# Kernel tuning notes

Measured on AMD Instinct MI355X. Metric: run time of the kernel, lower is better.

The kernel has to match this reference:

```python
import jax, jax.numpy as jnp
import numpy as np

N, M = 4096, 8192
NFEAT, EFEAT, NHID, NCLASS = 128, 64, 64, 16
ALPHA = 0.2
NEG = -9e15
BN_SCALE = np.float32(1.0 / np.sqrt(1.0 + 1e-5))  # eval BatchNorm: running stats (0,1), affine (1,0)


def _masked_att(hs, hd, a, mask):
    # hs: [P,F], hd: [Q,F], a: [2F], mask: [P,Q] binary
    F_ = hs.shape[1]
    logits = (hs @ a[:F_])[:, None] + (hd @ a[F_:])[None, :]            # [P,Q]
    logits = jnp.where(mask > 0, jax.nn.leaky_relu(logits, ALPHA), NEG)
    return jax.nn.softmax(logits, axis=1) @ hd                           # [P,F]


def _gat_layer(x, ex, adj, eadj, nem, Wn, We, ann, ane, aee, aen, concat):
    h = x @ Wn                                  # [N,F]
    g = ex @ We                                 # [M,F]
    Hn = _masked_att(h, h, ann, adj)            # node <- node neighbors
    He = _masked_att(h, g, ane, nem)            # node <- incident edges
    Ge = _masked_att(g, g, aee, eadj)           # edge <- adjacent edges
    Gn = _masked_att(g, h, aen, nem.T)          # edge <- endpoint nodes
    if concat:
        return (jax.nn.elu(jnp.concatenate([Hn, He], axis=1)),
                jax.nn.elu(jnp.concatenate([Ge, Gn], axis=1)))
    return Hn + He, Ge + Gn


def _mlp(h, W1, b1, W2, b2):
    h = jax.nn.relu((h @ W1 + b1) * BN_SCALE)
    return h @ W2 + b2


def _next_layer(h, A, W1, b1, W2, b2):
    pooled = A @ h                              # spmm(adj, h), dense-stored
    rep = _mlp(pooled, W1, b1, W2, b2)
    return jax.nn.relu(rep * BN_SCALE)


def setup_inputs() -> dict:
    key = jax.random.key(0)
    ks = jax.random.split(key, 40)
    f32 = jnp.float32
    x = jax.random.normal(ks[0], (N, NFEAT), f32)
    e_x = jax.random.normal(ks[1], (M, EFEAT), f32)
    adj = jnp.minimum((jax.random.uniform(ks[2], (N, N)) < 16.0 / N).astype(f32) + jnp.eye(N, dtype=f32), 1.0)
    e_adj = jnp.minimum((jax.random.uniform(ks[3], (M, M)) < 16.0 / M).astype(f32) + jnp.eye(M, dtype=f32), 1.0)
    n_e_adj = (jax.random.uniform(ks[4], (N, M)) < 4.0 / M).astype(f32)

    def lin(k, i, o):
        return jax.random.normal(k, (i, o), f32) * np.float32(1.0 / np.sqrt(i))

    def avec(k, F_):
        return jax.random.normal(k, (2 * F_,), f32) * np.float32(0.1)

    d = dict(x=x, e_x=e_x, adj=adj, e_adj=e_adj, n_e_adj=n_e_adj)
    # layer dims: (node_in, edge_in, out)
    dims = [(NFEAT, EFEAT, NHID), (2 * NHID, 2 * NHID, 2 * NHID), (64, 64, NCLASS)]
    ki = 5
    for li, (ni, ei, fo) in enumerate(dims):
        d[f'l{li}_Wn'] = lin(ks[ki], ni, fo); ki += 1
        d[f'l{li}_We'] = lin(ks[ki], ei, fo); ki += 1
        for nm in ('ann', 'ane', 'aee', 'aen'):
            d[f'l{li}_{nm}'] = avec(ks[ki], fo); ki += 1
    mdims = [(256, 64, 64), (64, 64, 64)]
    for mi, (i_, h_, o_) in enumerate(mdims):
        d[f'm{mi}_W1'] = lin(ks[ki], i_, h_); ki += 1
        d[f'm{mi}_b1'] = jnp.zeros((h_,), f32)
        d[f'm{mi}_W2'] = lin(ks[ki], h_, o_); ki += 1
        d[f'm{mi}_b2'] = jnp.zeros((o_,), f32)
    return d


def reference(x, e_x, adj, e_adj, n_e_adj,
              l0_Wn, l0_We, l0_ann, l0_ane, l0_aee, l0_aen,
              l1_Wn, l1_We, l1_ann, l1_ane, l1_aee, l1_aen,
              l2_Wn, l2_We, l2_ann, l2_ane, l2_aee, l2_aen,
              m0_W1, m0_b1, m0_W2, m0_b2,
              m1_W1, m1_b1, m1_W2, m1_b2):
    # dropout is identity in eval mode
    h, g = _gat_layer(x, e_x, adj, e_adj, n_e_adj, l0_Wn, l0_We, l0_ann, l0_ane, l0_aee, l0_aen, True)
    h, g = _gat_layer(h, g, adj, e_adj, n_e_adj, l1_Wn, l1_We, l1_ann, l1_ane, l1_aee, l1_aen, True)
    h_n, h_e = h, g
    h_n = _next_layer(h_n, adj, m0_W1, m0_b1, m0_W2, m0_b2)
    h_n = _next_layer(h_n, adj, m1_W1, m1_b1, m1_W2, m1_b2)
    h_e = _next_layer(h_e, e_adj, m0_W1, m0_b1, m0_W2, m0_b2)
    h_e = _next_layer(h_e, e_adj, m1_W1, m1_b1, m1_W2, m1_b2)
    fn, fe = _gat_layer(h_n, h_e, adj, e_adj, n_e_adj, l2_Wn, l2_We, l2_ann, l2_ane, l2_aee, l2_aen, False)
    return (jax.nn.log_softmax(jax.nn.elu(fn), axis=1),
            jax.nn.log_softmax(jax.nn.elu(fe), axis=1))
```

## Files before the change

### kernel.cpp

```cpp
#include <hip/hip_runtime.h>
#include <cmath>

constexpr int N_ = 4096;
constexpr int M_ = 8192;
constexpr float ALPHA_ = 0.2f;
constexpr float BN_SC = 0.9999950000374998f;
constexpr int CAP = 64;

typedef unsigned long long u64;

__device__ __forceinline__ float lrelu(float x) { return x > 0.f ? x : ALPHA_ * x; }
__device__ __forceinline__ float elu(float x) { return x > 0.f ? x : __expf(x) - 1.f; }

struct CsrA {
  const float* adj; const float* eadj; const float* nem;
  int* cA; int* iA; int* cE; int* iE; int* cN; int* iN; int* cT; int* iT;
};

__device__ void csr_body(const CsrA& a) {
  int wid = blockIdx.x * 8 + (threadIdx.x >> 6);
  int lane = threadIdx.x & 63;
  const float* mask; int row, Q; int* cnt; int* idx; bool tr = false;
  if (wid < N_)           { mask = a.adj;  row = wid;            Q = N_; cnt = a.cA; idx = a.iA; }
  else if (wid < N_ + M_) { mask = a.eadj; row = wid - N_;       Q = M_; cnt = a.cE; idx = a.iE; }
  else                    { mask = a.nem;  row = wid - N_ - M_;  Q = M_; cnt = a.cN; idx = a.iN; tr = true; }
  const float* mr = mask + (size_t)row * Q;
  u64 lt = (1ull << lane) - 1ull;
  int total = 0;
  for (int q0 = 0; q0 < Q; q0 += 256) {
    float4 v = *reinterpret_cast<const float4*>(mr + q0 + lane * 4);
    unsigned mk = (v.x > 0.5f ? 1u : 0u) | (v.y > 0.5f ? 2u : 0u) |
                  (v.z > 0.5f ? 4u : 0u) | (v.w > 0.5f ? 8u : 0u);
    u64 b0 = __ballot(mk & 1u), b1 = __ballot(mk & 2u), b2 = __ballot(mk & 4u), b3 = __ballot(mk & 8u);
    if (mk) {
      int base = total + __popcll(b0 & lt) + __popcll(b1 & lt) + __popcll(b2 & lt) + __popcll(b3 & lt);
      int ob = 0;
#pragma unroll
      for (int e = 0; e < 4; e++) {
        if (mk & (1u << e)) {
          int pos = base + ob;
          int j = q0 + lane * 4 + e;
          if (pos < CAP) idx[(size_t)row * CAP + pos] = j;
          if (tr) {
            int tp = atomicAdd(&a.cT[j], 1);
            if (tp < CAP) a.iT[(size_t)j * CAP + tp] = row;
          }
          ob++;
        }
      }
    }
    total += __popcll(b0) + __popcll(b1) + __popcll(b2) + __popcll(b3);
  }
  if (lane == 0) cnt[row] = min(total, CAP);
}

struct PDOp {
  const float* X; const float* W; int K, P;
  const float* a0; const float* a1; const float* a2; const float* a3;
  float* o0; float* o1; float* o2; float* o3;
  float* Y;
};

template <int F>
__device__ void proj_body(const PDOp& op, float* part) {
  constexpr int RPB = 512 / F;
  constexpr int KC = 8192 / F;
  __shared__ float Wl[8192];
  __shared__ float dred[8][4];
  int rl = threadIdx.x / F;
  int f = threadIdx.x % F;
  int p = blockIdx.x * RPB + rl;
  bool act = p < op.P;
  float acc = 0.f;
  for (int k0 = 0; k0 < op.K; k0 += KC) {
    int kc = min(KC, op.K - k0);
    __syncthreads();
    for (int i = threadIdx.x; i < kc * F; i += 512) Wl[i] = op.W[(size_t)k0 * F + i];
    __syncthreads();
    if (act) {
      const float4* xr4 = reinterpret_cast<const float4*>(op.X + (size_t)p * op.K + k0);
      for (int k = 0; k < kc; k += 4) {
        float4 xv = xr4[k >> 2];
        acc = fmaf(xv.x, Wl[k * F + f], acc);
        acc = fmaf(xv.y, Wl[(k + 1) * F + f], acc);
        acc = fmaf(xv.z, Wl[(k + 2) * F + f], acc);
        acc = fmaf(xv.w, Wl[(k + 3) * F + f], acc);
      }
    }
  }
  if (act) op.Y[(size_t)p * F + f] = acc;
  float q0 = acc * op.a0[f];
  float q1 = acc * op.a1[f];
  float q2 = acc * op.a2[f];
  float q3 = acc * op.a3[f];
  constexpr int WID = F < 64 ? F : 64;
#pragma unroll
  for (int t = 1; t < WID; t <<= 1) {
    q0 += __shfl_xor(q0, t, WID);
    q1 += __shfl_xor(q1, t, WID);
    q2 += __shfl_xor(q2, t, WID);
    q3 += __shfl_xor(q3, t, WID);
  }
  if constexpr (F == 128) {
    int w = threadIdx.x >> 6;
    if ((threadIdx.x & 63) == 0) { dred[w][0] = q0; dred[w][1] = q1; dred[w][2] = q2; dred[w][3] = q3; }
    __syncthreads();
    if (act && f == 0) {
      int w0 = rl * 2;
      op.o0[p] = dred[w0][0] + dred[w0 + 1][0];
      op.o1[p] = dred[w0][1] + dred[w0 + 1][1];
      op.o2[p] = dred[w0][2] + dred[w0 + 1][2];
      op.o3[p] = dred[w0][3] + dred[w0 + 1][3];
    }
  } else {
    if (act && f == 0) { op.o0[p] = q0; op.o1[p] = q1; op.o2[p] = q2; op.o3[p] = q3; }
  }
  float* sred = Wl;
  __syncthreads();
  sred[rl * F + f] = act ? acc : 0.f;
  __syncthreads();
  if (rl == 0) {
    float s = 0.f;
    for (int r = 0; r < RPB; r++) s += sred[r * F + f];
    part[(size_t)blockIdx.x * F + f] = s;
  }
}

__global__ __launch_bounds__(512) void phase0(CsrA ca, PDOp A, PDOp B,
                                              float* partH, float* partG) {
  if (blockIdx.y == 0) { csr_body(ca); return; }
  if (blockIdx.x >= 1024) return;
  if (blockIdx.y == 1) proj_body<64>(A, partH);
  else                 proj_body<64>(B, partG);
}

template <int F>
__global__ __launch_bounds__(512) void proj_l(PDOp A, PDOp B, float* partH, float* partG) {
  if (blockIdx.y == 0) proj_body<F>(A, partH);
  else                 proj_body<F>(B, partG);
}

template <int F>
__global__ __launch_bounds__(1024) void part_reduce(const float* __restrict__ partH,
                                                    const float* __restrict__ partG,
                                                    int nb,
                                                    float* __restrict__ oh, float* __restrict__ og) {
  constexpr int SL = 1024 / F;
  const float* part = blockIdx.y ? partG : partH;
  float* o = blockIdx.y ? og : oh;
  int f = threadIdx.x % F;
  int w = threadIdx.x / F;
  float s = 0.f;
  int b = w;
  for (; b + 8 * SL <= nb; b += 8 * SL) {
    float v0 = part[(size_t)(b + 0 * SL) * F + f];
    float v1 = part[(size_t)(b + 1 * SL) * F + f];
    float v2 = part[(size_t)(b + 2 * SL) * F + f];
    float v3 = part[(size_t)(b + 3 * SL) * F + f];
    float v4 = part[(size_t)(b + 4 * SL) * F + f];
    float v5 = part[(size_t)(b + 5 * SL) * F + f];
    float v6 = part[(size_t)(b + 6 * SL) * F + f];
    float v7 = part[(size_t)(b + 7 * SL) * F + f];
    s += ((v0 + v1) + (v2 + v3)) + ((v4 + v5) + (v6 + v7));
  }
  for (; b < nb; b += SL) s += part[(size_t)b * F + f];
  __shared__ float red[1024];
  red[threadIdx.x] = s;
  __syncthreads();
  if (w == 0) {
    float t = 0.f;
#pragma unroll
    for (int ww = 0; ww < SL; ww++) t += red[ww * F + f];
    o[f] = t;
  }
}

struct AOp {
  const int* cnt; int* idx; const float* s; const float* d;
  const float* Hd; const float* cs; float* out; int ldo, ocol, P, Q;
  int sortL; int* cTw;
};

template <int F>
__global__ __launch_bounds__(256) void att4(AOp A0, AOp A1, AOp A2, AOp A3) {
  int y = blockIdx.y;
  AOp op = y == 0 ? A0 : y == 1 ? A1 : y == 2 ? A2 : A3;
  constexpr int C = F / 64;
  int row = blockIdx.x * 4 + (threadIdx.x >> 6);
  int lane = threadIdx.x & 63;
  if (row >= op.P) return;
  int n = min(op.cnt[row], CAP);
  float acc[C];
  if (n == 0) {
    float invQ = 1.f / (float)op.Q;
#pragma unroll
    for (int c = 0; c < C; c++) acc[c] = op.cs[lane + c * 64] * invQ;
  } else {
    float sp = op.s[row];
    int* ip = op.idx + (size_t)row * CAP;
    int jl;
    if (op.sortL) {
      int v = lane < n ? ip[lane] : 0x7fffffff;
#pragma unroll
      for (int k = 2; k <= 64; k <<= 1) {
#pragma unroll
        for (int s = k >> 1; s > 0; s >>= 1) {
          int o = __shfl_xor(v, s);
          bool keepmin = (((lane & s) == 0) == ((lane & k) == 0));
          v = keepmin ? min(v, o) : max(v, o);
        }
      }
      if (lane < n) ip[lane] = v;
      if (lane == 0) op.cTw[row] = n;
      jl = lane < n ? v : 0;
    } else {
      jl = lane < n ? ip[lane] : 0;
    }
    float dl = lane < n ? op.d[jl] : -INFINITY;
    float mm = dl;
#pragma unroll
    for (int t = 1; t < 64; t <<= 1) mm = fmaxf(mm, __shfl_xor(mm, t));
    float m = lrelu(sp + mm);
    float el = lane < n ? __expf(lrelu(sp + dl) - m) : 0.f;
    float l = el;
#pragma unroll
    for (int t = 1; t < 64; t <<= 1) l += __shfl_xor(l, t);
    float invl = 1.f / l;
#pragma unroll
    for (int c = 0; c < C; c++) acc[c] = 0.f;
    int k = 0;
    for (; k + 2 <= n; k += 2) {
      int j0 = __shfl(jl, k), j1 = __shfl(jl, k + 1);
      float e0 = __shfl(el, k), e1 = __shfl(el, k + 1);
      const float* h0 = op.Hd + (size_t)j0 * F + lane;
      const float* h1 = op.Hd + (size_t)j1 * F + lane;
#pragma unroll
      for (int c = 0; c < C; c++) acc[c] = fmaf(e0, h0[c * 64], fmaf(e1, h1[c * 64], acc[c]));
    }
    if (k < n) {
      int j0 = __shfl(jl, k);
      float e0 = __shfl(el, k);
#pragma unroll
      for (int c = 0; c < C; c++) acc[c] = fmaf(e0, op.Hd[(size_t)j0 * F + lane + c * 64], acc[c]);
    }
#pragma unroll
    for (int c = 0; c < C; c++) acc[c] *= invl;
  }
  float* o = op.out + (size_t)row * op.ldo + op.ocol + lane;
#pragma unroll
  for (int c = 0; c < C; c++) o[c * 64] = elu(acc[c]);
}

template <int C>
__global__ __launch_bounds__(256) void nextlayer(
    const int* __restrict__ cA, const int* __restrict__ iA,
    const int* __restrict__ cE, const int* __restrict__ iE,
    const float* __restrict__ HdN, const float* __restrict__ HdM,
    const float* __restrict__ W1, const float* __restrict__ b1,
    const float* __restrict__ W2, const float* __restrict__ b2,
    float* __restrict__ outN, float* __restrict__ outM) {
  constexpr int KD = C * 64;
  int y = blockIdx.y;
  const int* cnt = y ? cE : cA;
  const int* idx = y ? iE : iA;
  const float* Hd = y ? HdM : HdN;
  float* out = y ? outM : outN;
  int P = y ? M_ : N_;
  int w = threadIdx.x >> 6, lane = threadIdx.x & 63;
  int row = blockIdx.x * 4 + w;
  if (row >= P) return;
  int n = min(cnt[row], CAP);
  const int* ip = idx + (size_t)row * CAP;
  int jl = lane < n ? ip[lane] : 0;
  float acc[C];
#pragma unroll
  for (int c = 0; c < C; c++) acc[c] = 0.f;
  int k = 0;
  for (; k + 2 <= n; k += 2) {
    int j0 = __shfl(jl, k), j1 = __shfl(jl, k + 1);
    const float* h0 = Hd + (size_t)j0 * KD + lane;
    const float* h1 = Hd + (size_t)j1 * KD + lane;
#pragma unroll
    for (int c = 0; c < C; c++) acc[c] += h0[c * 64] + h1[c * 64];
  }
  if (k < n) {
    int j0 = __shfl(jl, k);
#pragma unroll
    for (int c = 0; c < C; c++) acc[c] += Hd[(size_t)j0 * KD + lane + c * 64];
  }
  float y1 = 0.f;
#pragma unroll
  for (int c = 0; c < C; c++) {
    for (int kk = 0; kk < 64; kk++)
      y1 = fmaf(__shfl(acc[c], kk), W1[(c * 64 + kk) * 64 + lane], y1);
  }
  y1 = fmaxf((y1 + b1[lane]) * BN_SC, 0.f);
  float y2 = 0.f;
  for (int kk = 0; kk < 64; kk++)
    y2 = fmaf(__shfl(y1, kk), W2[kk * 64 + lane], y2);
  out[(size_t)row * 64 + lane] = fmaxf((y2 + b2[lane]) * BN_SC, 0.f);
}

__device__ __forceinline__ float att_col16(const int* cnt, const int* idx, float sp,
                                           const float* d, const float* Hd,
                                           const float* cs, int Q, int row, int c) {
  int n = min(cnt[row], CAP);
  if (n == 0) return cs[c] / (float)Q;
  const int* ip = idx + (size_t)row * CAP;
  float mm = -INFINITY;
  for (int k0 = 0; k0 < n; k0 += 16) {
    int k = k0 + c;
    float dv = k < n ? d[ip[k]] : -INFINITY;
    mm = fmaxf(mm, dv);
  }
#pragma unroll
  for (int t = 1; t < 16; t <<= 1) mm = fmaxf(mm, __shfl_xor(mm, t, 16));
  float m = lrelu(sp + mm);
  float l = 0.f, a = 0.f;
  for (int k0 = 0; k0 < n; k0 += 16) {
    int k = k0 + c;
    int jx = k < n ? ip[k] : 0;
    float dv = k < n ? d[jx] : 0.f;
    float ex = k < n ? __expf(lrelu(sp + dv) - m) : 0.f;
    int kmax = min(16, n - k0);
    for (int kk = 0; kk < kmax; kk++) {
      float e = __shfl(ex, kk, 16);
      int j = __shfl(jx, kk, 16);
      l += e;
      a = fmaf(e, Hd[(size_t)j * 16 + c], a);
    }
  }
  return a / l;
}

__global__ __launch_bounds__(256) void att_final(
    const int* __restrict__ cA, const int* __restrict__ iA, const float* __restrict__ s0, const float* __restrict__ d0,
    const int* __restrict__ cN, const int* __restrict__ iN, const float* __restrict__ s1, const float* __restrict__ d1,
    const int* __restrict__ cE, const int* __restrict__ iE, const float* __restrict__ s2, const float* __restrict__ d2,
    const int* __restrict__ cT, const int* __restrict__ iT, const float* __restrict__ s3, const float* __restrict__ d3,
    const float* __restrict__ h2, const float* __restrict__ g2,
    const float* __restrict__ csh, const float* __restrict__ csg,
    float* __restrict__ out) {
  int y = blockIdx.y;
  int gid = blockIdx.x * 256 + threadIdx.x;
  int row = gid >> 4, c = gid & 15;
  float v; float* dst;
  if (y == 0) {
    if (row >= N_) return;
    v = att_col16(cA, iA, s0[row], d0, h2, csh, N_, row, c)
      + att_col16(cN, iN, s1[row], d1, g2, csg, M_, row, c);
    dst = out + (size_t)row * 16 + c;
  } else {
    if (row >= M_) return;
    v = att_col16(cE, iE, s2[row], d2, g2, csg, M_, row, c)
      + att_col16(cT, iT, s3[row], d3, h2, csh, N_, row, c);
    dst = out + (size_t)(N_ + row) * 16 + c;
  }
  v = elu(v);
  float mx = v;
#pragma unroll
  for (int t = 1; t < 16; t <<= 1) mx = fmaxf(mx, __shfl_xor(mx, t, 16));
  float ex = __expf(v - mx);
  float sm = ex;
#pragma unroll
  for (int t = 1; t < 16; t <<= 1) sm += __shfl_xor(sm, t, 16);
  *dst = v - mx - __logf(sm);
}

extern "C" void kernel_launch(void* const* d_in, const int* in_sizes, int n_in,
                              void* d_out, int out_size, void* d_ws, size_t ws_size,
                              hipStream_t stream) {
  (void)in_sizes; (void)n_in; (void)out_size; (void)ws_size;
  const float* x    = (const float*)d_in[0];
  const float* e_x  = (const float*)d_in[1];
  const float* adj  = (const float*)d_in[2];
  const float* eadj = (const float*)d_in[3];
  const float* nem  = (const float*)d_in[4];
  const float* l_Wn[3]  = {(const float*)d_in[5],  (const float*)d_in[11], (const float*)d_in[17]};
  const float* l_We[3]  = {(const float*)d_in[6],  (const float*)d_in[12], (const float*)d_in[18]};
  const float* l_ann[3] = {(const float*)d_in[7],  (const float*)d_in[13], (const float*)d_in[19]};
  const float* l_ane[3] = {(const float*)d_in[8],  (const float*)d_in[14], (const float*)d_in[20]};
  const float* l_aee[3] = {(const float*)d_in[9],  (const float*)d_in[15], (const float*)d_in[21]};
  const float* l_aen[3] = {(const float*)d_in[10], (const float*)d_in[16], (const float*)d_in[22]};
  const float* m_W1[2] = {(const float*)d_in[23], (const float*)d_in[27]};
  const float* m_b1[2] = {(const float*)d_in[24], (const float*)d_in[28]};
  const float* m_W2[2] = {(const float*)d_in[25], (const float*)d_in[29]};
  const float* m_b2[2] = {(const float*)d_in[26], (const float*)d_in[30]};
  float* outp = (float*)d_out;

  char* wsp = (char*)d_ws;
  size_t off = 0;
  auto alloc = [&](size_t bytes) -> void* {
    void* p = wsp + off;
    off += (bytes + 255) & ~(size_t)255;
    return p;
  };
  int* cT = (int*)alloc((size_t)M_ * 4);
  size_t zero_bytes = off;

  float* bufH = (float*)alloc((size_t)2048 * 128 * 4);
  float* bufG = (float*)alloc((size_t)2048 * 128 * 4);
  float* csh = (float*)alloc(3 * 128 * 4);
  float* csg = (float*)alloc(3 * 128 * 4);

  int* cA = (int*)alloc((size_t)N_ * 4);
  int* cE = (int*)alloc((size_t)M_ * 4);
  int* cN = (int*)alloc((size_t)N_ * 4);
  int* iA = (int*)alloc((size_t)N_ * CAP * 4);
  int* iE = (int*)alloc((size_t)M_ * CAP * 4);
  int* iN = (int*)alloc((size_t)N_ * CAP * 4);
  int* iT = (int*)alloc((size_t)M_ * CAP * 4);

  float* ht  = (float*)alloc((size_t)N_ * 128 * 4);
  float* gt  = (float*)alloc((size_t)M_ * 128 * 4);
  float* hA  = (float*)alloc((size_t)N_ * 128 * 4);
  float* gA  = (float*)alloc((size_t)M_ * 128 * 4);
  float* hB  = (float*)alloc((size_t)N_ * 256 * 4);
  float* gB  = (float*)alloc((size_t)M_ * 256 * 4);
  float* h64a = (float*)alloc((size_t)N_ * 64 * 4);
  float* g64a = (float*)alloc((size_t)M_ * 64 * 4);
  float* h64b = (float*)alloc((size_t)N_ * 64 * 4);
  float* g64b = (float*)alloc((size_t)M_ * 64 * 4);
  float* h16 = (float*)alloc((size_t)N_ * 16 * 4);
  float* g16 = (float*)alloc((size_t)M_ * 16 * 4);
  float* s0N = (float*)alloc((size_t)N_ * 4);
  float* d0N = (float*)alloc((size_t)N_ * 4);
  float* s1N = (float*)alloc((size_t)N_ * 4);
  float* d3N = (float*)alloc((size_t)N_ * 4);
  float* d1M = (float*)alloc((size_t)M_ * 4);
  float* s2M = (float*)alloc((size_t)M_ * 4);
  float* d2M = (float*)alloc((size_t)M_ * 4);
  float* s3M = (float*)alloc((size_t)M_ * 4);

  dim3 B(256);
  hipMemsetAsync(wsp, 0, zero_bytes, stream);

  auto mkH = [&](int F, const float* Xh, int Kh, float* Yh, int li) {
    return PDOp{Xh, l_Wn[li], Kh, N_, l_ann[li], l_ann[li] + F, l_ane[li], l_aen[li] + F,
                s0N, d0N, s1N, d3N, Yh};
  };
  auto mkG = [&](int F, const float* Xg, int Kg, float* Yg, int li) {
    return PDOp{Xg, l_We[li], Kg, M_, l_ane[li] + F, l_aee[li], l_aee[li] + F, l_aen[li],
                d1M, s2M, d2M, s3M, Yg};
  };

  {
    CsrA ca{adj, eadj, nem, cA, iA, cE, iE, cN, iN, cT, iT};
    phase0<<<dim3(2048, 3), dim3(512), 0, stream>>>(
        ca, mkH(64, x, 128, ht, 0), mkG(64, e_x, 64, gt, 0), bufH, bufG);
  }
  part_reduce<64><<<dim3(1, 2), dim3(1024), 0, stream>>>(bufH, bufG, 1024, csh + 0, csg + 0);

  att4<64><<<dim3(M_ / 4, 4), B, 0, stream>>>(
      AOp{cA, iA, s0N, d0N, ht, csh + 0, hA, 128, 0, N_, N_, 0, nullptr},
      AOp{cN, iN, s1N, d1M, gt, csg + 0, hA, 128, 64, N_, M_, 0, nullptr},
      AOp{cE, iE, s2M, d2M, gt, csg + 0, gA, 128, 0, M_, M_, 0, nullptr},
      AOp{cT, iT, s3M, d3N, ht, csh + 0, gA, 128, 64, M_, N_, 1, cT});

  proj_l<128><<<dim3(2048, 2), dim3(512), 0, stream>>>(
      mkH(128, hA, 128, ht, 1), mkG(128, gA, 128, gt, 1), bufH, bufG);
  part_reduce<128><<<dim3(1, 2), dim3(1024), 0, stream>>>(bufH, bufG, 2048, csh + 128, csg + 128);
  att4<128><<<dim3(M_ / 4, 4), B, 0, stream>>>(
      AOp{cA, iA, s0N, d0N, ht, csh + 128, hB, 256, 0, N_, N_, 0, nullptr},
      AOp{cN, iN, s1N, d1M, gt, csg + 128, hB, 256, 128, N_, M_, 0, nullptr},
      AOp{cE, iE, s2M, d2M, gt, csg + 128, gB, 256, 0, M_, M_, 0, nullptr},
      AOp{cT, iT, s3M, d3N, ht, csh + 128, gB, 256, 128, M_, N_, 0, nullptr});

  nextlayer<4><<<dim3(M_ / 4, 2), B, 0, stream>>>(cA, iA, cE, iE, hB, gB,
      m_W1[0], m_b1[0], m_W2[0], m_b2[0], h64a, g64a);
  nextlayer<1><<<dim3(M_ / 4, 2), B, 0, stream>>>(cA, iA, cE, iE, h64a, g64a,
      m_W1[1], m_b1[1], m_W2[1], m_b2[1], h64b, g64b);

  proj_l<16><<<dim3(256, 2), dim3(512), 0, stream>>>(
      mkH(16, h64b, 64, h16, 2), mkG(16, g64b, 64, g16, 2), bufH, bufG);
  part_reduce<16><<<dim3(1, 2), dim3(1024), 0, stream>>>(bufH, bufG, 256, csh + 256, csg + 256);
  att_final<<<dim3(M_ * 16 / 256, 2), B, 0, stream>>>(
      cA, iA, s0N, d0N, cN, iN, s1N, d1M, cE, iE, s2M, d2M, cT, iT, s3M, d3N,
      h16, g16, csh + 256, csg + 256, outp);
}
```

Before: 325.7 us.

## Split CSR build into grid-stride bit-packing pass and bitmap-scan kernel

The dense mask-to-CSR conversion, which ran one wavefront per row with per-chunk ballots, is replaced by two stages. First, a grid-stride pass in phase0 packs each float mask into a 1-bit-per-entry bitmap using wide coalesced loads. Second, a separate kernel scans the bitmaps with popcount and a wavefront prefix sum to emit neighbour indices. This aims to keep the dense-mask read bandwidth-bound and parallel instead of latency-bound per row, at the cost of an extra launch and a bitmap buffer round trip.

```diff
diff --git a/kernel.cpp b/kernel.cpp
--- a/kernel.cpp
+++ b/kernel.cpp
@@ -8,48 +8,67 @@
 constexpr int CAP = 64;
 
 typedef unsigned long long u64;
+typedef unsigned short u16;
 
 __device__ __forceinline__ float lrelu(float x) { return x > 0.f ? x : ALPHA_ * x; }
 __device__ __forceinline__ float elu(float x) { return x > 0.f ? x : __expf(x) - 1.f; }
 
-struct CsrA {
-  const float* adj; const float* eadj; const float* nem;
-  int* cA; int* iA; int* cE; int* iE; int* cN; int* iN; int* cT; int* iT;
-};
-
-__device__ void csr_body(const CsrA& a) {
-  int wid = blockIdx.x * 8 + (threadIdx.x >> 6);
+__device__ void pack_body(const float* __restrict__ m, u64* __restrict__ bits, int nw16) {
+  int stride = 2048 * 512;
+  u16* out = reinterpret_cast<u16*>(bits);
+  for (int w = blockIdx.x * 512 + threadIdx.x; w < nw16; w += stride) {
+    const float4* p = reinterpret_cast<const float4*>(m) + (size_t)w * 4;
+    float4 v0 = p[0], v1 = p[1], v2 = p[2], v3 = p[3];
+    unsigned mk =
+        (v0.x > 0.5f ? 1u : 0u)      | (v0.y > 0.5f ? 2u : 0u)      |
+        (v0.z > 0.5f ? 4u : 0u)      | (v0.w > 0.5f ? 8u : 0u)      |
+        (v1.x > 0.5f ? 16u : 0u)     | (v1.y > 0.5f ? 32u : 0u)     |
+        (v1.z > 0.5f ? 64u : 0u)     | (v1.w > 0.5f ? 128u : 0u)    |
+        (v2.x > 0.5f ? 256u : 0u)    | (v2.y > 0.5f ? 512u : 0u)    |
+        (v2.z > 0.5f ? 1024u : 0u)   | (v2.w > 0.5f ? 2048u : 0u)   |
+        (v3.x > 0.5f ? 4096u : 0u)   | (v3.y > 0.5f ? 8192u : 0u)   |
+        (v3.z > 0.5f ? 16384u : 0u)  | (v3.w > 0.5f ? 32768u : 0u);
+    out[w] = (u16)mk;
+  }
+}
+
+__global__ __launch_bounds__(256) void csr_bits(
+    const u64* __restrict__ bA, const u64* __restrict__ bE, const u64* __restrict__ bN,
+    int* __restrict__ cA, int* __restrict__ iA,
+    int* __restrict__ cE, int* __restrict__ iE,
+    int* __restrict__ cN, int* __restrict__ iN,
+    int* __restrict__ cT, int* __restrict__ iT) {
+  int wid = blockIdx.x * 4 + (threadIdx.x >> 6);
   int lane = threadIdx.x & 63;
-  const float* mask; int row, Q; int* cnt; int* idx; bool tr = false;
-  if (wid < N_)           { mask = a.adj;  row = wid;            Q = N_; cnt = a.cA; idx = a.iA; }
-  else if (wid < N_ + M_) { mask = a.eadj; row = wid - N_;       Q = M_; cnt = a.cE; idx = a.iE; }
-  else                    { mask = a.nem;  row = wid - N_ - M_;  Q = M_; cnt = a.cN; idx = a.iN; tr = true; }
-  const float* mr = mask + (size_t)row * Q;
-  u64 lt = (1ull << lane) - 1ull;
+  const u64* bits; int row, Qw; int* cnt; int* idx; bool tr = false;
+  if (wid < N_)           { bits = bA; row = wid;            Qw = N_ / 64; cnt = cA; idx = iA; }
+  else if (wid < N_ + M_) { bits = bE; row = wid - N_;       Qw = M_ / 64; cnt = cE; idx = iE; }
+  else                    { bits = bN; row = wid - N_ - M_;  Qw = M_ / 64; cnt = cN; idx = iN; tr = true; }
+  const u64* br = bits + (size_t)row * Qw;
   int total = 0;
-  for (int q0 = 0; q0 < Q; q0 += 256) {
-    float4 v = *reinterpret_cast<const float4*>(mr + q0 + lane * 4);
-    unsigned mk = (v.x > 0.5f ? 1u : 0u) | (v.y > 0.5f ? 2u : 0u) |
-                  (v.z > 0.5f ? 4u : 0u) | (v.w > 0.5f ? 8u : 0u);
-    u64 b0 = __ballot(mk & 1u), b1 = __ballot(mk & 2u), b2 = __ballot(mk & 4u), b3 = __ballot(mk & 8u);
-    if (mk) {
-      int base = total + __popcll(b0 & lt) + __popcll(b1 & lt) + __popcll(b2 & lt) + __popcll(b3 & lt);
-      int ob = 0;
-#pragma unroll
-      for (int e = 0; e < 4; e++) {
-        if (mk & (1u << e)) {
-          int pos = base + ob;
-          int j = q0 + lane * 4 + e;
-          if (pos < CAP) idx[(size_t)row * CAP + pos] = j;
-          if (tr) {
-            int tp = atomicAdd(&a.cT[j], 1);
-            if (tp < CAP) a.iT[(size_t)j * CAP + tp] = row;
-          }
-          ob++;
-        }
+  for (int w0 = 0; w0 < Qw; w0 += 64) {
+    u64 b = br[w0 + lane];
+    int c = __popcll(b);
+    int pre = c;
+#pragma unroll
+    for (int t = 1; t < 64; t <<= 1) {
+      int o = __shfl_up(pre, t);
+      if (lane >= t) pre += o;
+    }
+    int base = total + pre - c;
+    int jbase = (w0 + lane) * 64;
+    while (b) {
+      int bit = __ffsll(b) - 1;
+      b &= b - 1;
+      int j = jbase + bit;
+      if (base < CAP) idx[(size_t)row * CAP + base] = j;
+      if (tr) {
+        int tp = atomicAdd(&cT[j], 1);
+        if (tp < CAP) iT[(size_t)j * CAP + tp] = row;
       }
-    }
-    total += __popcll(b0) + __popcll(b1) + __popcll(b2) + __popcll(b3);
+      base++;
+    }
+    total += __shfl(pre, 63);
   }
   if (lane == 0) cnt[row] = min(total, CAP);
 }
@@ -126,9 +145,16 @@
   }
 }
 
-__global__ __launch_bounds__(512) void phase0(CsrA ca, PDOp A, PDOp B,
-                                              float* partH, float* partG) {
-  if (blockIdx.y == 0) { csr_body(ca); return; }
+__global__ __launch_bounds__(512) void phase0(
+    const float* adj, const float* eadj, const float* nem,
+    u64* bA, u64* bE, u64* bN,
+    PDOp A, PDOp B, float* partH, float* partG) {
+  if (blockIdx.y == 0) {
+    pack_body(adj, bA, N_ * N_ / 16);
+    pack_body(eadj, bE, M_ * M_ / 16);
+    pack_body(nem, bN, N_ * M_ / 16);
+    return;
+  }
   if (blockIdx.x >= 1024) return;
   if (blockIdx.y == 1) proj_body<64>(A, partH);
   else                 proj_body<64>(B, partG);
@@ -398,6 +424,10 @@
   int* cT = (int*)alloc((size_t)M_ * 4);
   size_t zero_bytes = off;
 
+  u64* bA = (u64*)alloc((size_t)N_ * (N_ / 64) * 8);
+  u64* bE = (u64*)alloc((size_t)M_ * (M_ / 64) * 8);
+  u64* bN = (u64*)alloc((size_t)N_ * (M_ / 64) * 8);
+
   float* bufH = (float*)alloc((size_t)2048 * 128 * 4);
   float* bufG = (float*)alloc((size_t)2048 * 128 * 4);
   float* csh = (float*)alloc(3 * 128 * 4);
@@ -444,12 +474,13 @@
                 d1M, s2M, d2M, s3M, Yg};
   };
 
-  {
-    CsrA ca{adj, eadj, nem, cA, iA, cE, iE, cN, iN, cT, iT};
-    phase0<<<dim3(2048, 3), dim3(512), 0, stream>>>(
-        ca, mkH(64, x, 128, ht, 0), mkG(64, e_x, 64, gt, 0), bufH, bufG);
-  }
+  phase0<<<dim3(2048, 3), dim3(512), 0, stream>>>(
+      adj, eadj, nem, bA, bE, bN,
+      mkH(64, x, 128, ht, 0), mkG(64, e_x, 64, gt, 0), bufH, bufG);
   part_reduce<64><<<dim3(1, 2), dim3(1024), 0, stream>>>(bufH, bufG, 1024, csh + 0, csg + 0);
+
+  csr_bits<<<dim3((2 * N_ + M_) / 4), B, 0, stream>>>(bA, bE, bN,
+                                                      cA, iA, cE, iE, cN, iN, cT, iT);
 
   att4<64><<<dim3(M_ / 4, 4), B, 0, stream>>>(
       AOp{cA, iA, s0N, d0N, ht, csh + 0, hA, 128, 0, N_, N_, 0, nullptr},
```

Measured after the change: 327.0 us. About the same (+0.4%).
